# Kernel optimization log

Measured on AMD Instinct MI355X. Metric: run time of the kernel, lower is better.

## Reference

```python
import jax, jax.numpy as jnp
import numpy as np

HEADS = 4
PATCH = 32
KSIZE = 5


def conv2d(x, w, groups=1):
    return jax.lax.conv_general_dilated(
        x, w, (1, 1), 'SAME', feature_group_count=groups,
        dimension_numbers=('NCHW', 'OIHW', 'NCHW'))


def window_starts(size, step, d):
    return [min(i, size - d) for i in range(0, size + step - d, step)]


def local_partition(x, tops, lefts, dh, dw):
    wins = [x[:, :, t:t + dh, l:l + dw] for t in tops for l in lefts]
    return jnp.stack(wins, axis=1)  # (b, nwin, c, dh, dw)


def local_reverse(local_x, shape, tops, lefts, dh, dw):
    b, c, h, w = shape
    out = jnp.zeros(shape, local_x.dtype)
    cnt = jnp.zeros((h, w), local_x.dtype)
    idx = 0
    for t in tops:
        for l in lefts:
            out = out.at[:, :, t:t + dh, l:l + dw].add(local_x[:, idx])
            cnt = cnt.at[t:t + dh, l:l + dw].add(1.0)
            idx += 1
    out = out / cnt  # broadcast over (b, c)
    return jnp.nan_to_num(out, nan=1e-5, posinf=1e-5, neginf=1e-5)


def dynamic_filtering(x, w1, w2, ks):
    # x: (b, c, t, h, w); conv3d kernels have size 1 in t -> per-frame 2D conv
    b, c, t, h, w = x.shape
    y = x.transpose(0, 2, 1, 3, 4).reshape(b * t, c, h, w)
    f = conv2d(y, w1)
    f = jnp.where(f >= 0, f, 0.2 * f)  # LeakyReLU(0.2)
    ker = conv2d(f, w2).reshape(b, t, ks * ks, h, w)
    K = t * ks * ks
    # rearrange 'b (k1 k2) t h w -> b h w (t k1 k2)' then normalize over last dim
    kerf = ker.transpose(0, 3, 4, 1, 2).reshape(b, h, w, K)
    kerf = kerf - jnp.mean(kerf, axis=-1, keepdims=True) + 1.0 / K
    kern = kerf.reshape(b, h, w, t, ks * ks).transpose(0, 3, 4, 1, 2)  # (b,t,kk,h,w)
    p = (ks - 1) // 2
    xp = jnp.pad(x, ((0, 0), (0, 0), (0, 0), (p, p), (p, p)), mode='edge')
    out = jnp.zeros((b, c, h, w), x.dtype)
    for ti in range(t):  # small fixed loops (t*ks*ks taps) instead of full unfold
        for kk in range(ks * ks):
            di, dj = kk // ks, kk % ks
            out = out + xp[:, :, ti, di:di + h, dj:dj + w] * kern[:, ti, kk][:, None]
    return out


def forward(x, k_cached, v_cached, W_qkv, W_dw, W_f1, W_f2, W_proj, temperature):
    b, c, h, w = x.shape
    ph = pw = PATCH
    qkv = jnp.einsum('oc,bchw->bohw', W_qkv, x)          # 1x1 conv
    qkv = conv2d(qkv, W_dw, groups=3 * c)                 # 3x3 depthwise
    q, k, v = jnp.split(qkv, 3, axis=1)
    k_ = jnp.concatenate([k_cached, k[:, :, None]], axis=2)
    v_ = jnp.concatenate([v_cached, k[:, :, None]], axis=2)  # faithful to source (uses k, not v)
    k = dynamic_filtering(k_, W_f1, W_f2, KSIZE)
    v = dynamic_filtering(v_, W_f1, W_f2, KSIZE)
    tops = window_starts(h, h - ph // 4, ph)
    lefts = window_starts(w, w - pw // 4, pw)
    nwin = len(tops) * len(lefts)
    ch = c // HEADS

    def split_heads(t):
        loc = local_partition(t, tops, lefts, ph, pw)  # (b,nwin,c,ph,pw)
        return loc.reshape(b * nwin, HEADS, ch, ph * pw).transpose(0, 1, 3, 2)

    qh, kh, vh = split_heads(q), split_heads(k), split_heads(v)
    qh = qh / jnp.maximum(jnp.linalg.norm(qh, axis=-1, keepdims=True), 1e-12)
    kh = kh / jnp.maximum(jnp.linalg.norm(kh, axis=-1, keepdims=True), 1e-12)
    attn = jnp.einsum('nhsc,nhtc->nhst', qh, kh) * temperature  # temperature (H,1,1)
    attn = jax.nn.softmax(attn, axis=-1)
    oh = jnp.einsum('nhst,nhtc->nhsc', attn, vh)
    loc = oh.transpose(0, 1, 3, 2).reshape(b, nwin, c, ph, pw)
    out = local_reverse(loc, (b, c, h, w), tops, lefts, ph, pw)
    out = jnp.einsum('oc,bchw->bohw', W_proj, out)        # 1x1 conv
    return out, k_[:, :, -2:], v_[:, :, -2:]


def setup_inputs() -> dict:
    key = jax.random.key(0)
    ks = jax.random.split(key, 8)
    d = 64
    return {
        'x': jax.random.normal(ks[0], (8, d, 64, 64), jnp.float32),
        'k_cached': jax.random.normal(ks[1], (8, d, 1, 64, 64), jnp.float32),
        'v_cached': jax.random.normal(ks[2], (8, d, 1, 64, 64), jnp.float32),
        'W_qkv': 0.05 * jax.random.normal(ks[3], (3 * d, d), jnp.float32),
        'W_dw': 0.05 * jax.random.normal(ks[4], (3 * d, 1, 3, 3), jnp.float32),
        'W_f1': 0.05 * jax.random.normal(ks[5], (d, d, 3, 3), jnp.float32),
        'W_f2': 0.05 * jax.random.normal(ks[6], (KSIZE * KSIZE, d, 3, 3), jnp.float32),
        'W_proj': 0.05 * jax.random.normal(ks[7], (d, d), jnp.float32),
        'temperature': jnp.ones((HEADS, 1, 1), jnp.float32),
    }


def reference(x, k_cached, v_cached, W_qkv, W_dw, W_f1, W_f2, W_proj, temperature):
    return forward(x, k_cached, v_cached, W_qkv, W_dw, W_f1, W_f2, W_proj, temperature)
```

## Files before the change

### kernel.cpp

```cpp
#include <hip/hip_runtime.h>
#include <math.h>

#define B_ 8
#define C_ 64
#define HW_ 4096

#define OUT_N   2097152
#define KV_N    4194304

typedef short s4v __attribute__((ext_vector_type(4)));
typedef short s8v __attribute__((ext_vector_type(8)));
typedef float f4v __attribute__((ext_vector_type(4)));
typedef unsigned int u2v __attribute__((ext_vector_type(2)));
typedef unsigned short ushort_t;

__device__ inline unsigned short f2bf(float f) {
    unsigned int u = __builtin_bit_cast(unsigned int, f);
    u += 0x7FFFu + ((u >> 16) & 1u);
    return (unsigned short)(u >> 16);
}

__device__ inline unsigned int bfpack_t(float a, float b) {
    unsigned int ua = __builtin_bit_cast(unsigned int, a);
    unsigned int ub = __builtin_bit_cast(unsigned int, b);
    return __builtin_amdgcn_perm(ub, ua, 0x07060302u);
}

#define MFMA16(a, b, c) __builtin_amdgcn_mfma_f32_16x16x16bf16_1k(a, b, c, 0, 0, 0)
#define LO4(v) __builtin_shufflevector(v, v, 0, 1, 2, 3)
#define HI4(v) __builtin_shufflevector(v, v, 4, 5, 6, 7)

__global__ __launch_bounds__(256) void k0_copy(const float* __restrict__ kc,
                                               const float* __restrict__ vc,
                                               float* __restrict__ k_out,
                                               float* __restrict__ v_out) {
    int i = blockIdx.x * 256 + threadIdx.x;
    const int n = B_ * C_ * HW_;
    int which = (i >= n);
    int j = which ? i - n : i;
    int bc = j >> 12, hw = j & 4095;
    const float* src = which ? vc : kc;
    float* dst = which ? v_out : k_out;
    dst[((size_t)bc * 2) * HW_ + hw] = src[j];
}

__global__ __launch_bounds__(256) void wprep(const float* __restrict__ Wf1,
                                             const float* __restrict__ Wf2,
                                             ushort_t* __restrict__ wt1,
                                             ushort_t* __restrict__ wt2) {
    int id = blockIdx.x * 256 + threadIdx.x;
    if (id >= 6912) return;
    ushort_t o[8];
    if (id < 4608) {
        int lane = id & 63; int p = (id >> 6) % 18; int ocg = id / (18 * 64);
        int tap = p >> 1, m = p & 1;
        int oc = ocg * 16 + (lane & 15);
        int ic0 = m * 32 + (lane >> 4) * 8;
#pragma unroll
        for (int j = 0; j < 8; ++j)
            o[j] = f2bf(Wf1[((size_t)oc * 64 + ic0 + j) * 9 + tap]);
        *(uint4*)(wt1 + (size_t)id * 8) = *(uint4*)o;
    } else {
        int id2 = id - 4608;
        int lane = id2 & 63; int p = (id2 >> 6) % 18; int ocg = id2 / (18 * 64);
        int tap = p >> 1, m = p & 1;
        int oc = ocg * 16 + (lane & 15);
        int ic0 = m * 32 + (lane >> 4) * 8;
#pragma unroll
        for (int j = 0; j < 8; ++j)
            o[j] = (oc < 25) ? f2bf(Wf2[((size_t)oc * 64 + ic0 + j) * 9 + tap]) : (ushort_t)0;
        *(uint4*)(wt2 + (size_t)id2 * 8) = *(uint4*)o;
    }
}

__global__ __launch_bounds__(256) void k1_mfma(const float* __restrict__ x,
                                               const float* __restrict__ Wqkv,
                                               float* __restrict__ qkv) {
    int blk = blockIdx.x;
    int tid = threadIdx.x, lane = tid & 63, wv = tid >> 6;
    int px0 = (blk & 15) * 256 + wv * 64;
    int otile = (blk >> 4) & 7, b = blk >> 7;
    int ln15 = lane & 15, g4 = (lane >> 4) * 4;

    const float* xb = x + (size_t)b * 64 * HW_;
    s4v wf[4];
#pragma unroll
    for (int k = 0; k < 4; ++k) {
        const float* wr = Wqkv + (size_t)(otile * 16 + ln15) * 64 + k * 16 + g4;
        float4 w4 = *(const float4*)wr;
        u2v u; u.x = bfpack_t(w4.x, w4.y); u.y = bfpack_t(w4.z, w4.w);
        wf[k] = __builtin_bit_cast(s4v, u);
    }
    const f4v zf = {0.f, 0.f, 0.f, 0.f};
    f4v acc[4] = {zf, zf, zf, zf};
#pragma unroll
    for (int k = 0; k < 4; ++k) {
#pragma unroll
        for (int p = 0; p < 4; ++p) {
            const float* xp = xb + (size_t)(k * 16 + g4) * HW_ + px0 + p * 16 + ln15;
            float v0 = xp[0];
            float v1 = xp[HW_];
            float v2 = xp[2 * HW_];
            float v3 = xp[3 * HW_];
            u2v u; u.x = bfpack_t(v0, v1); u.y = bfpack_t(v2, v3);
            s4v xf = __builtin_bit_cast(s4v, u);
            acc[p] = MFMA16(wf[k], xf, acc[p]);
        }
    }
    float* ob = qkv + ((size_t)b * 128 + otile * 16) * HW_ + px0;
#pragma unroll
    for (int p = 0; p < 4; ++p)
#pragma unroll
        for (int j = 0; j < 4; ++j)
            ob[(size_t)(g4 + j) * HW_ + p * 16 + ln15] = acc[p][j];
}

__global__ __launch_bounds__(256) void k2_dw(const float* __restrict__ qkv,
                                             const float* __restrict__ Wdw,
                                             float* __restrict__ qbuf,
                                             float* __restrict__ k_out,
                                             float* __restrict__ v_out) {
    int t = blockIdx.x * 256 + threadIdx.x;
    int hw = t & 4095; int bo = t >> 12; int o = bo & 127; int b = bo >> 7;
    int y = hw >> 6, xx0 = hw & 63;
    const float* in = qkv + (size_t)bo * HW_;
    const float* w = Wdw + o * 9;
    float acc = 0.f;
#pragma unroll
    for (int dy = 0; dy < 3; ++dy) {
        int yy = y + dy - 1;
        if (yy < 0 || yy > 63) continue;
#pragma unroll
        for (int dx = 0; dx < 3; ++dx) {
            int xx = xx0 + dx - 1;
            if (xx < 0 || xx > 63) continue;
            acc = fmaf(in[yy * 64 + xx], w[dy * 3 + dx], acc);
        }
    }
    if (o < 64) {
        qbuf[((size_t)b * 64 + o) * HW_ + hw] = acc;
    } else {
        int oc = o - 64;
        size_t off = (((size_t)b * 64 + oc) * 2 + 1) * HW_ + hw;
        k_out[off] = acc;
        v_out[off] = acc;
    }
}

__global__ __launch_bounds__(256) void k3_mfma1(const float* __restrict__ k_out,
                                                const float* __restrict__ vc,
                                                const ushort_t* __restrict__ wt1,
                                                ushort_t* __restrict__ fb16) {
    int stripe = blockIdx.x;
    int f = blockIdx.y;
    int tid = threadIdx.x;
    __shared__ ushort_t ilds[4 * 66 * 72];
    const float* src; size_t icstr;
    if (f < 16) { src = k_out + (((size_t)(f >> 1) * 128) + (f & 1)) * HW_; icstr = 2 * HW_; }
    else        { src = vc + ((size_t)(f - 16) * 64) * HW_;                 icstr = HW_; }
    int y0 = stripe * 2;

    int lane = tid & 63, wv = tid >> 6, g = lane >> 4, c16 = lane & 15;
    s8v a[18];
    const ushort_t* wb = wt1 + ((size_t)wv * 18) * 512 + lane * 8;
#pragma unroll
    for (int p = 0; p < 18; ++p) a[p] = *(const s8v*)(wb + p * 512);

    {
        int rc = tid >> 5, idx = tid & 31;
        int r = rc >> 1, side = rc & 1;
        ((unsigned int*)ilds)[(r * 66 + side * 65) * 36 + idx] = 0u;
    }
    {
        int r = tid >> 6, x = tid & 63;
        int y = y0 - 1 + r;
        bool valid = (y >= 0 && y < 64);
        const float* rowp = src + y * 64 + x;
        ushort_t* dst = ilds + ((r * 66) + x + 1) * 72;
#pragma unroll
        for (int ic4 = 0; ic4 < 16; ++ic4) {
            ushort_t o[4];
#pragma unroll
            for (int j = 0; j < 4; ++j) {
                float v = valid ? rowp[(size_t)(ic4 * 4 + j) * icstr] : 0.f;
                o[j] = f2bf(v);
            }
            *(uint2*)(dst + ic4 * 4) = *(uint2*)o;
        }
    }
    __syncthreads();

#pragma unroll
    for (int r_out = 0; r_out < 2; ++r_out)
#pragma unroll
        for (int xp = 0; xp < 2; ++xp) {
            int x0 = xp * 32, x1 = x0 + 16;
            f4v acc0 = {0.f, 0.f, 0.f, 0.f}, acc1 = {0.f, 0.f, 0.f, 0.f};
#pragma unroll
            for (int tap = 0; tap < 9; ++tap) {
                const int dy = tap / 3, dx = tap % 3;
                const ushort_t* bp0 = ilds + (((r_out + dy) * 66) + x0 + c16 + dx) * 72 + g * 8;
                const ushort_t* bp1 = ilds + (((r_out + dy) * 66) + x1 + c16 + dx) * 72 + g * 8;
                s8v b00 = *(const s8v*)bp0;
                s8v b01 = *(const s8v*)(bp0 + 32);
                s8v b10 = *(const s8v*)bp1;
                s8v b11 = *(const s8v*)(bp1 + 32);
                acc0 = MFMA16(LO4(a[2 * tap]),     LO4(b00), acc0);
                acc1 = MFMA16(LO4(a[2 * tap]),     LO4(b10), acc1);
                acc0 = MFMA16(HI4(a[2 * tap]),     HI4(b00), acc0);
                acc1 = MFMA16(HI4(a[2 * tap]),     HI4(b10), acc1);
                acc0 = MFMA16(LO4(a[2 * tap + 1]), LO4(b01), acc0);
                acc1 = MFMA16(LO4(a[2 * tap + 1]), LO4(b11), acc1);
                acc0 = MFMA16(HI4(a[2 * tap + 1]), HI4(b01), acc0);
                acc1 = MFMA16(HI4(a[2 * tap + 1]), HI4(b11), acc1);
            }
            int py = (y0 + r_out) * 64;
#pragma unroll
            for (int j = 0; j < 4; ++j) {
                int oc = wv * 16 + g * 4 + j;
                float v0 = acc0[j]; v0 = (v0 >= 0.f) ? v0 : 0.2f * v0;
                float v1 = acc1[j]; v1 = (v1 >= 0.f) ? v1 : 0.2f * v1;
                fb16[((size_t)f * 64 + oc) * HW_ + py + x0 + c16] = f2bf(v0);
                fb16[((size_t)f * 64 + oc) * HW_ + py + x1 + c16] = f2bf(v1);
            }
        }
}

__global__ __launch_bounds__(256) void k3b_mfma2(const ushort_t* __restrict__ fb16,
                                                 const ushort_t* __restrict__ wt2,
                                                 float* __restrict__ kerb) {
    int stripe = blockIdx.x;
    int f = blockIdx.y;
    int tid = threadIdx.x;
    __shared__ ushort_t ilds[4 * 66 * 72];
    int y0 = stripe * 2;

    int lane = tid & 63, wv = tid >> 6, g = lane >> 4, c16 = lane & 15;
    int ocg = wv & 1, xh = wv >> 1;
    s8v a[18];
    const ushort_t* wb = wt2 + ((size_t)ocg * 18) * 512 + lane * 8;
#pragma unroll
    for (int p = 0; p < 18; ++p) a[p] = *(const s8v*)(wb + p * 512);

    {
        int rc = tid >> 5, idx = tid & 31;
        int r = rc >> 1, side = rc & 1;
        ((unsigned int*)ilds)[(r * 66 + side * 65) * 36 + idx] = 0u;
    }
    {
        int r = tid >> 6, x = tid & 63;
        int y = y0 - 1 + r;
        bool valid = (y >= 0 && y < 64);
        const ushort_t* rowp = fb16 + (size_t)f * 64 * HW_ + y * 64 + x;
        ushort_t* dst = ilds + ((r * 66) + x + 1) * 72;
#pragma unroll
        for (int ic4 = 0; ic4 < 16; ++ic4) {
            ushort_t o[4];
#pragma unroll
            for (int j = 0; j < 4; ++j)
                o[j] = valid ? rowp[(size_t)(ic4 * 4 + j) * HW_] : (ushort_t)0;
            *(uint2*)(dst + ic4 * 4) = *(uint2*)o;
        }
    }
    __syncthreads();

#pragma unroll
    for (int r_out = 0; r_out < 2; ++r_out) {
        int x0 = xh * 32, x1 = x0 + 16;
        f4v acc0 = {0.f, 0.f, 0.f, 0.f}, acc1 = {0.f, 0.f, 0.f, 0.f};
#pragma unroll
        for (int tap = 0; tap < 9; ++tap) {
            const int dy = tap / 3, dx = tap % 3;
            const ushort_t* bp0 = ilds + (((r_out + dy) * 66) + x0 + c16 + dx) * 72 + g * 8;
            const ushort_t* bp1 = ilds + (((r_out + dy) * 66) + x1 + c16 + dx) * 72 + g * 8;
            s8v b00 = *(const s8v*)bp0;
            s8v b01 = *(const s8v*)(bp0 + 32);
            s8v b10 = *(const s8v*)bp1;
            s8v b11 = *(const s8v*)(bp1 + 32);
            acc0 = MFMA16(LO4(a[2 * tap]),     LO4(b00), acc0);
            acc1 = MFMA16(LO4(a[2 * tap]),     LO4(b10), acc1);
            acc0 = MFMA16(HI4(a[2 * tap]),     HI4(b00), acc0);
            acc1 = MFMA16(HI4(a[2 * tap]),     HI4(b10), acc1);
            acc0 = MFMA16(LO4(a[2 * tap + 1]), LO4(b01), acc0);
            acc1 = MFMA16(LO4(a[2 * tap + 1]), LO4(b11), acc1);
            acc0 = MFMA16(HI4(a[2 * tap + 1]), HI4(b01), acc0);
            acc1 = MFMA16(HI4(a[2 * tap + 1]), HI4(b11), acc1);
        }
        int py = (y0 + r_out) * 64;
#pragma unroll
        for (int j = 0; j < 4; ++j) {
            int oc = ocg * 16 + g * 4 + j;
            if (oc < 25) {
                kerb[((size_t)f * 25 + oc) * HW_ + py + x0 + c16] = acc0[j];
                kerb[((size_t)f * 25 + oc) * HW_ + py + x1 + c16] = acc1[j];
            }
        }
    }
}

__global__ __launch_bounds__(256) void k4b_apply(const float* __restrict__ kerb,
                                                 const float* __restrict__ k_out,
                                                 const float* __restrict__ v_out,
                                                 float* __restrict__ kfil,
                                                 float* __restrict__ vfil) {
    int y = blockIdx.x, b = blockIdx.y;
    int p = blockIdx.z >> 1, chh = blockIdx.z & 1;
    int tid = threadIdx.x;
    __shared__ float klds[50][64];
    __shared__ float part[4][64];
    int f0 = (p == 0) ? 2 * b : 16 + b;
    int f1 = 2 * b + 1;
    for (int idx = tid; idx < 3200; idx += 256) {
        int px_ = idx & 63, j = idx >> 6;
        int ti = (j >= 25); int kk = j - ti * 25;
        int fr = ti ? f1 : f0;
        klds[j][px_] = kerb[((size_t)fr * 25 + kk) * HW_ + y * 64 + px_];
    }
    __syncthreads();
    {
        int px_ = tid & 63, q_ = tid >> 6;
        int j0 = q_ * 13; int j1 = j0 + 13; if (j1 > 50) j1 = 50;
        float s = 0.f;
        for (int j = j0; j < j1; ++j) s += klds[j][px_];
        part[q_][px_] = s;
    }
    __syncthreads();
    if (tid < 64) {
        float m = (part[0][tid] + part[1][tid]) + (part[2][tid] + part[3][tid]);
        part[0][tid] = m * (1.f / 50.f);
    }
    __syncthreads();
    for (int idx = tid; idx < 3200; idx += 256) {
        int px_ = idx & 63, j = idx >> 6;
        klds[j][px_] += 0.02f - part[0][px_];
    }
    __syncthreads();

    int px = tid & 63, cq = tid >> 6;
    const float* xsrc = ((p == 0) ? k_out : v_out)
                      + (size_t)b * 64 * 2 * HW_ + (size_t)chh * 32 * 2 * HW_;
    float acc[8];
#pragma unroll
    for (int i = 0; i < 8; ++i) acc[i] = 0.f;

#pragma unroll
    for (int ti = 0; ti < 2; ++ti) {
        for (int kk = 0; kk < 25; ++kk) {
            int cy = y + kk / 5 - 2;  cy = cy < 0 ? 0 : (cy > 63 ? 63 : cy);
            int cx = px + kk % 5 - 2; cx = cx < 0 ? 0 : (cx > 63 ? 63 : cx);
            float kv = klds[ti * 25 + kk][px];
            const float* xb = xsrc + (size_t)ti * HW_ + cy * 64 + cx;
#pragma unroll
            for (int i = 0; i < 8; ++i)
                acc[i] = fmaf(xb[(size_t)(cq + 4 * i) * 2 * HW_], kv, acc[i]);
        }
    }
    float* ob = ((p == 0) ? kfil : vfil)
              + ((size_t)b * 64 + chh * 32) * HW_ + y * 64 + px;
#pragma unroll
    for (int i = 0; i < 8; ++i) ob[(size_t)(cq + 4 * i) * HW_] = acc[i];
}

__global__ __launch_bounds__(256) void k4c_cvt(const float* __restrict__ qbuf,
                                               const float* __restrict__ kfil,
                                               unsigned short* __restrict__ qbf,
                                               unsigned short* __restrict__ kbf) {
    int row = blockIdx.x * 256 + threadIdx.x;
    int unit = blockIdx.y;
    int which = blockIdx.z;
    int win = unit & 3, head = (unit >> 2) & 3, b = unit >> 4;
    int wy = win >> 1, wx = win & 1;
    int gpx = ((wy * 32 + (row >> 5)) << 6) + wx * 32 + (row & 31);
    const float* src = (which ? kfil : qbuf) + ((size_t)b * 64 + head * 16) * HW_ + gpx;
    float v[16]; float ss = 0.f;
#pragma unroll
    for (int i = 0; i < 16; ++i) { v[i] = src[(size_t)i * HW_]; ss = fmaf(v[i], v[i], ss); }
    float sc = 1.f / fmaxf(sqrtf(ss), 1e-12f);
    unsigned short o[16];
#pragma unroll
    for (int i = 0; i < 16; ++i) o[i] = f2bf(v[i] * sc);
    unsigned short* dst = (which ? kbf : qbf) + ((size_t)unit * 1024 + row) * 16;
    ((uint4*)dst)[0] = ((uint4*)o)[0];
    ((uint4*)dst)[1] = ((uint4*)o)[1];
}

__global__ __launch_bounds__(256) void k5_mfma(const unsigned short* __restrict__ qbf,
                                               const unsigned short* __restrict__ kbf,
                                               const float* __restrict__ vfil,
                                               const float* __restrict__ temp,
                                               float* __restrict__ attno) {
    int qb = blockIdx.x;
    int unit = blockIdx.y;
    int win = unit & 3, head = (unit >> 2) & 3, b = unit >> 4;
    int wy = win >> 1, wx = win & 1;
    int tid = threadIdx.x, lane = tid & 63, wv = tid >> 6;
    __shared__ unsigned short vt[16][1032];
    size_t cbase = ((size_t)b * 64 + head * 16) * HW_;

#pragma unroll
    for (int it = 0; it < 4; ++it) {
        int i = it * 256 + tid;
        int ch = i >> 6, k16 = (i & 63) << 4;
        int gpx = ((wy * 32 + (k16 >> 5)) << 6) + wx * 32 + (k16 & 31);
        const float* src = vfil + cbase + (size_t)ch * HW_ + gpx;
        unsigned int w[8];
#pragma unroll
        for (int j = 0; j < 8; ++j) w[j] = bfpack_t(src[2 * j], src[2 * j + 1]);
        uint4* d = (uint4*)&vt[ch][k16];
        d[0] = *(uint4*)&w[0];
        d[1] = *(uint4*)&w[4];
    }

    float tmp = temp[head];
    float a_s = tmp * 1.44269504f;
    float b_s = (fabsf(tmp) + 1e-6f) * 1.44269504f;

    int ln15 = lane & 15, g4 = (lane >> 4) * 4;
    const unsigned short* qu = qbf + (size_t)unit * 1024 * 16;
    const unsigned short* ku = kbf + (size_t)unit * 1024 * 16;
    int qt0 = qb * 8 + wv * 2;
    s4v qf0 = *(const s4v*)(qu + ((size_t)(qt0 * 16 + ln15)) * 16 + g4);
    s4v qf1 = *(const s4v*)(qu + ((size_t)((qt0 + 1) * 16 + ln15)) * 16 + g4);

    const short one_bf = (short)0x3F80;
    const s4v ones = {one_bf, one_bf, one_bf, one_bf};
    const f4v zf = {0.f, 0.f, 0.f, 0.f};
    f4v o0 = zf, o1 = zf, lacc0 = zf, lacc1 = zf;

    __syncthreads();
    for (int tb = 0; tb < 64; ++tb) {
        s4v kf = *(const s4v*)(ku + ((size_t)(tb * 16 + ln15)) * 16 + g4);
        s4v vf = *(const s4v*)(&vt[ln15][tb * 16 + g4]);
        f4v s0 = MFMA16(kf, qf0, zf);
        f4v s1 = MFMA16(kf, qf1, zf);
        float p00 = __builtin_amdgcn_exp2f(fmaf(s0[0], a_s, -b_s));
        float p01 = __builtin_amdgcn_exp2f(fmaf(s0[1], a_s, -b_s));
        float p02 = __builtin_amdgcn_exp2f(fmaf(s0[2], a_s, -b_s));
        float p03 = __builtin_amdgcn_exp2f(fmaf(s0[3], a_s, -b_s));
        float p10 = __builtin_amdgcn_exp2f(fmaf(s1[0], a_s, -b_s));
        float p11 = __builtin_amdgcn_exp2f(fmaf(s1[1], a_s, -b_s));
        float p12 = __builtin_amdgcn_exp2f(fmaf(s1[2], a_s, -b_s));
        float p13 = __builtin_amdgcn_exp2f(fmaf(s1[3], a_s, -b_s));
        u2v u0; u0.x = bfpack_t(p00, p01); u0.y = bfpack_t(p02, p03);
        u2v u1; u1.x = bfpack_t(p10, p11); u1.y = bfpack_t(p12, p13);
        s4v pf0 = __builtin_bit_cast(s4v, u0);
        s4v pf1 = __builtin_bit_cast(s4v, u1);
        o0 = MFMA16(vf, pf0, o0);
        o1 = MFMA16(vf, pf1, o1);
        lacc0 = MFMA16(ones, pf0, lacc0);
        lacc1 = MFMA16(ones, pf1, lacc1);
    }

    float inv0 = 1.f / lacc0[0], inv1 = 1.f / lacc1[0];

    int q0 = qt0 * 16 + ln15;
    int q1 = q0 + 16;
    int gq0 = ((wy * 32 + (q0 >> 5)) << 6) + wx * 32 + (q0 & 31);
    int gq1 = ((wy * 32 + (q1 >> 5)) << 6) + wx * 32 + (q1 & 31);
#pragma unroll
    for (int j = 0; j < 4; ++j) {
        attno[cbase + (size_t)(g4 + j) * HW_ + gq0] = o0[j] * inv0;
        attno[cbase + (size_t)(g4 + j) * HW_ + gq1] = o1[j] * inv1;
    }
}

__global__ __launch_bounds__(256) void k6_mfma(const float* __restrict__ attno,
                                               const float* __restrict__ Wp,
                                               float* __restrict__ out) {
    int blk = blockIdx.x;
    int tid = threadIdx.x, lane = tid & 63, wv = tid >> 6;
    int px0 = (blk & 15) * 256 + wv * 64;
    int otile = (blk >> 4) & 3, b = blk >> 6;
    int ln15 = lane & 15, g4 = (lane >> 4) * 4;

    const float* ab = attno + (size_t)b * 64 * HW_;
    s4v wf[4];
#pragma unroll
    for (int k = 0; k < 4; ++k) {
        const float* wr = Wp + (size_t)(otile * 16 + ln15) * 64 + k * 16 + g4;
        float4 w4 = *(const float4*)wr;
        u2v u; u.x = bfpack_t(w4.x, w4.y); u.y = bfpack_t(w4.z, w4.w);
        wf[k] = __builtin_bit_cast(s4v, u);
    }
    const f4v zf = {0.f, 0.f, 0.f, 0.f};
    f4v acc[4] = {zf, zf, zf, zf};
#pragma unroll
    for (int k = 0; k < 4; ++k) {
#pragma unroll
        for (int p = 0; p < 4; ++p) {
            const float* xp = ab + (size_t)(k * 16 + g4) * HW_ + px0 + p * 16 + ln15;
            float v0 = xp[0];
            float v1 = xp[HW_];
            float v2 = xp[2 * HW_];
            float v3 = xp[3 * HW_];
            u2v u; u.x = bfpack_t(v0, v1); u.y = bfpack_t(v2, v3);
            s4v xf = __builtin_bit_cast(s4v, u);
            acc[p] = MFMA16(wf[k], xf, acc[p]);
        }
    }
    float* ob = out + ((size_t)b * 64 + otile * 16) * HW_ + px0;
#pragma unroll
    for (int p = 0; p < 4; ++p)
#pragma unroll
        for (int j = 0; j < 4; ++j)
            ob[(size_t)(g4 + j) * HW_ + p * 16 + ln15] = acc[p][j];
}

extern "C" void kernel_launch(void* const* d_in, const int* in_sizes, int n_in,
                              void* d_out, int out_size, void* d_ws, size_t ws_size,
                              hipStream_t stream) {
    const float* x    = (const float*)d_in[0];
    const float* kc   = (const float*)d_in[1];
    const float* vc   = (const float*)d_in[2];
    const float* Wqkv = (const float*)d_in[3];
    const float* Wdw  = (const float*)d_in[4];
    const float* Wf1  = (const float*)d_in[5];
    const float* Wf2  = (const float*)d_in[6];
    const float* Wpr  = (const float*)d_in[7];
    const float* temp = (const float*)d_in[8];

    float* out   = (float*)d_out;
    float* k_out = out + OUT_N;
    float* v_out = out + OUT_N + KV_N;

    float* ws   = (float*)d_ws;
    float* qkv  = ws;
    unsigned short* fb16 = (unsigned short*)ws;
    unsigned short* qbf = (unsigned short*)ws;
    unsigned short* kbf = (unsigned short*)(ws + 1048576);
    float* qbuf = ws + 6291456;
    float* kerb = ws + 8388608;
    float* kfil = ws + 10846208;
    float* vfil = ws + 12943360;
    unsigned short* wt1 = (unsigned short*)(ws + 15106048);
    unsigned short* wt2 = wt1 + 36864;
    float* attno= kerb;

    wprep   <<<27,    256, 0, stream>>>(Wf1, Wf2, wt1, wt2);
    k0_copy <<<16384, 256, 0, stream>>>(kc, vc, k_out, v_out);
    k1_mfma <<<1024,  256, 0, stream>>>(x, Wqkv, qkv);
    k2_dw   <<<16384, 256, 0, stream>>>(qkv, Wdw, qbuf, k_out, v_out);
    k3_mfma1<<<dim3(32, 24), 256, 0, stream>>>(k_out, vc, wt1, fb16);
    k3b_mfma2<<<dim3(32, 24), 256, 0, stream>>>(fb16, wt2, kerb);
    k4b_apply<<<dim3(64, 8, 4), 256, 0, stream>>>(kerb, k_out, v_out, kfil, vfil);
    k4c_cvt <<<dim3(4, 128, 2), 256, 0, stream>>>(qbuf, kfil, qbf, kbf);
    k5_mfma <<<dim3(8, 128), 256, 0, stream>>>(qbf, kbf, vfil, temp, attno);
    k6_mfma <<<512,   256, 0, stream>>>(attno, Wpr, out);
}
```

Before: 178.4 us.

## Register-tile dynamic filter: 4 pixels x 2 channels per thread with float4 row loads

Each thread of the dynamic-filtering stage now computes 4 adjacent pixels for 2 channels instead of one pixel for 8 channels. For each of the five kernel rows it loads a 12-wide window with float4 reads and reuses it across the five horizontal taps, handling edge clamping with selects. Filter taps are read from LDS as float4 and outputs are written as float4. The aim is fewer scalar global loads and less address arithmetic, in exchange for more registers per thread.

```diff
diff --git a/kernel.cpp b/kernel.cpp
--- a/kernel.cpp
+++ b/kernel.cpp
@@ -336,29 +336,64 @@
     }
     __syncthreads();
 
-    int px = tid & 63, cq = tid >> 6;
+    int pg = tid & 15, cg = tid >> 4;
+    int px4 = pg * 4;
     const float* xsrc = ((p == 0) ? k_out : v_out)
-                      + (size_t)b * 64 * 2 * HW_ + (size_t)chh * 32 * 2 * HW_;
-    float acc[8];
-#pragma unroll
-    for (int i = 0; i < 8; ++i) acc[i] = 0.f;
+                      + ((size_t)b * 64 + chh * 32 + cg * 2) * 2 * HW_;
+    float acc0[4] = {0.f, 0.f, 0.f, 0.f};
+    float acc1[4] = {0.f, 0.f, 0.f, 0.f};
+    bool ledge = (px4 == 0), redge = (px4 == 60);
+    int loff = ledge ? 0 : px4 - 4;
+    int roff = redge ? 60 : px4 + 4;
 
 #pragma unroll
     for (int ti = 0; ti < 2; ++ti) {
-        for (int kk = 0; kk < 25; ++kk) {
-            int cy = y + kk / 5 - 2;  cy = cy < 0 ? 0 : (cy > 63 ? 63 : cy);
-            int cx = px + kk % 5 - 2; cx = cx < 0 ? 0 : (cx > 63 ? 63 : cx);
-            float kv = klds[ti * 25 + kk][px];
-            const float* xb = xsrc + (size_t)ti * HW_ + cy * 64 + cx;
-#pragma unroll
-            for (int i = 0; i < 8; ++i)
-                acc[i] = fmaf(xb[(size_t)(cq + 4 * i) * 2 * HW_], kv, acc[i]);
+#pragma unroll
+        for (int r = 0; r < 5; ++r) {
+            int cy = y + r - 2; cy = cy < 0 ? 0 : (cy > 63 ? 63 : cy);
+            const float* sp0 = xsrc + (size_t)ti * HW_ + cy * 64;
+            const float* sp1 = sp0 + 2 * HW_;
+            float xw0[12], xw1[12];
+            {
+                float4 l4 = *(const float4*)(sp0 + loff);
+                float4 m4 = *(const float4*)(sp0 + px4);
+                float4 r4 = *(const float4*)(sp0 + roff);
+                xw0[0] = l4.x; xw0[1] = l4.y;
+                xw0[2] = ledge ? l4.x : l4.z;
+                xw0[3] = ledge ? l4.x : l4.w;
+                xw0[4] = m4.x; xw0[5] = m4.y; xw0[6] = m4.z; xw0[7] = m4.w;
+                xw0[8] = redge ? r4.w : r4.x;
+                xw0[9] = redge ? r4.w : r4.y;
+                xw0[10] = r4.z; xw0[11] = r4.w;
+            }
+            {
+                float4 l4 = *(const float4*)(sp1 + loff);
+                float4 m4 = *(const float4*)(sp1 + px4);
+                float4 r4 = *(const float4*)(sp1 + roff);
+                xw1[0] = l4.x; xw1[1] = l4.y;
+                xw1[2] = ledge ? l4.x : l4.z;
+                xw1[3] = ledge ? l4.x : l4.w;
+                xw1[4] = m4.x; xw1[5] = m4.y; xw1[6] = m4.z; xw1[7] = m4.w;
+                xw1[8] = redge ? r4.w : r4.x;
+                xw1[9] = redge ? r4.w : r4.y;
+                xw1[10] = r4.z; xw1[11] = r4.w;
+            }
+#pragma unroll
+            for (int dx = 0; dx < 5; ++dx) {
+                float4 kv = *(const float4*)&klds[ti * 25 + r * 5 + dx][px4];
+                float kva[4] = {kv.x, kv.y, kv.z, kv.w};
+#pragma unroll
+                for (int i = 0; i < 4; ++i) {
+                    acc0[i] = fmaf(xw0[i + dx + 2], kva[i], acc0[i]);
+                    acc1[i] = fmaf(xw1[i + dx + 2], kva[i], acc1[i]);
+                }
+            }
         }
     }
     float* ob = ((p == 0) ? kfil : vfil)
-              + ((size_t)b * 64 + chh * 32) * HW_ + y * 64 + px;
-#pragma unroll
-    for (int i = 0; i < 8; ++i) ob[(size_t)(cq + 4 * i) * HW_] = acc[i];
+              + ((size_t)b * 64 + chh * 32 + cg * 2) * HW_ + y * 64 + px4;
+    *(float4*)ob = *(float4*)acc0;
+    *(float4*)(ob + HW_) = *(float4*)acc1;
 }
 
 __global__ __launch_bounds__(256) void k4c_cvt(const float* __restrict__ qbuf,
```

Result: slower. 184.8 us (+3.6%).
